# Performance work log

Measured on AMD Instinct MI355X. Metric: run time of the kernel, lower is better.

Reference implementation:

```python
import jax, jax.numpy as jnp
import numpy as np

IN_C, OUT_C, K, N_FILTERS, STRIDE, PAD = 256, 512, 3, 64, 1, 1


def setup_inputs() -> dict:
    key = jax.random.key(0)
    kx, kw, kb, krw, krb = jax.random.split(key, 5)
    fan_in = IN_C * K * K
    bound = 1.0 / np.sqrt(fan_in)
    x = jax.random.normal(kx, (32, IN_C, 56, 56), dtype=jnp.float32)
    weight = jax.random.uniform(kw, (OUT_C, IN_C, K, K), minval=-bound, maxval=bound, dtype=jnp.float32)
    bias = jax.random.uniform(kb, (OUT_C,), minval=-bound, maxval=bound, dtype=jnp.float32)
    rbound = 1.0 / np.sqrt(IN_C)
    router_w = jax.random.uniform(krw, (OUT_C, IN_C), minval=-rbound, maxval=rbound, dtype=jnp.float32)
    router_b = jax.random.uniform(krb, (OUT_C,), minval=-rbound, maxval=rbound, dtype=jnp.float32)
    return {"x": x, "weight": weight, "bias": bias, "router_w": router_w, "router_b": router_b}


def reference(x, weight, bias, router_w, router_b):
    B = x.shape[0]
    # router: global avg pool -> linear -> top-k channel mask
    pooled = jnp.mean(x, axis=(2, 3))                      # [B, IN_C]
    router_out = pooled @ router_w.T + router_b            # [B, OUT_C]
    _, top_idx = jax.lax.top_k(router_out, N_FILTERS)      # [B, k]
    mask = jnp.zeros((B, OUT_C), dtype=x.dtype).at[jnp.arange(B)[:, None], top_idx].set(1.0)
    # dense conv2d
    conv = jax.lax.conv_general_dilated(
        x, weight, window_strides=(STRIDE, STRIDE), padding=[(PAD, PAD), (PAD, PAD)],
        dimension_numbers=("NCHW", "OIHW", "NCHW"))
    conv = conv + bias[None, :, None, None]
    return conv * mask[:, :, None, None]
```

## Files before the change

### kernel.cpp

```cpp
#include <hip/hip_runtime.h>

#define IN_C   256
#define OUT_C  512
#define WIDTH  56
#define HW     3136
#define KTOT   2304
#define NF     64
#define NU     448
#define NB     32
#define NGRP   8
#define TN     64
#define NTILE  49
#define SROWS  192

typedef __bf16 bf16x8 __attribute__((ext_vector_type(8)));
typedef float  f32x4  __attribute__((ext_vector_type(4)));

__global__ __launch_bounds__(256) void xpose_kernel(const float* __restrict__ x,
                                                    __bf16* __restrict__ xT,
                                                    float* __restrict__ partial) {
    int id = blockIdx.x;
    int b = id / NTILE, tile = id - b * NTILE;
    int ptile = tile * TN;
    int tid = threadIdx.x;
    __shared__ float tl[64][65];
    __shared__ float plsum[IN_C];
    const float* xb  = x + (size_t)b * IN_C * HW + ptile;
    __bf16*      xtb = xT + ((size_t)b * HW + ptile) * IN_C;
    int pxq  = tid & 15;
    int rowi = tid >> 4;
    int px   = tid >> 2;
    int icq  = tid & 3;
    for (int chunk = 0; chunk < 4; ++chunk) {
        #pragma unroll
        for (int r = 0; r < 4; ++r) {
            int icL = r * 16 + rowi;
            int ic  = chunk * 64 + icL;
            float4 v = *(const float4*)(xb + (size_t)ic * HW + pxq * 4);
            *(float4*)&tl[icL][pxq * 4] = v;
            float s = v.x + v.y + v.z + v.w;
            s += __shfl_down(s, 8, 16);
            s += __shfl_down(s, 4, 16);
            s += __shfl_down(s, 2, 16);
            s += __shfl_down(s, 1, 16);
            if (pxq == 0) plsum[ic] = s;
        }
        __syncthreads();
        bf16x8 o0, o1;
        #pragma unroll
        for (int k = 0; k < 8; ++k) o0[k] = (__bf16)tl[icq * 16 + k][px];
        #pragma unroll
        for (int k = 0; k < 8; ++k) o1[k] = (__bf16)tl[icq * 16 + 8 + k][px];
        __bf16* dst = xtb + (size_t)px * IN_C + chunk * 64 + icq * 16;
        *(bf16x8*)dst = o0;
        *(bf16x8*)(dst + 8) = o1;
        __syncthreads();
    }
    partial[(size_t)id * IN_C + tid] = plsum[tid];
}

__global__ __launch_bounds__(256) void wfrag_kernel(const float* __restrict__ w,
                                                    __bf16* __restrict__ wf) {
    int oc = blockIdx.x;
    __shared__ float sm[KTOT];
    const float* src = w + (size_t)oc * KTOT;
    int tid = threadIdx.x;
    #pragma unroll
    for (int k = 0; k < 9; ++k) sm[k * 256 + tid] = src[k * 256 + tid];
    __syncthreads();
    __bf16* dst = wf + (size_t)oc * KTOT;
    for (int C = tid; C < 288; C += 256) {
        int d0  = C * 8;
        int icg = d0 / 288;
        int rem = d0 - icg * 288;
        int tap = rem >> 5, icl0 = rem & 31;
        bf16x8 o;
        #pragma unroll
        for (int j = 0; j < 8; ++j)
            o[j] = (__bf16)sm[(icg * 32 + icl0 + j) * 9 + tap];
        *(bf16x8*)&dst[d0] = o;
    }
}

__global__ __launch_bounds__(512) void router_kernel(const float* __restrict__ partial,
                                                     const float* __restrict__ rw,
                                                     const float* __restrict__ rb,
                                                     int* __restrict__ sel,
                                                     int* __restrict__ unsel) {
    int b = blockIdx.x;
    __shared__ float p[IN_C];
    __shared__ float v[OUT_C];
    __shared__ int   scount, ucount;
    int t = threadIdx.x;
    if (t < IN_C) {
        float s = 0.f;
        const float* pb = partial + (size_t)b * NTILE * IN_C + t;
        for (int k = 0; k < NTILE; ++k) s += pb[k * IN_C];
        p[t] = s * (1.0f / HW);
    }
    if (t == 0) { scount = 0; ucount = 0; }
    __syncthreads();
    int w = t >> 6, lane = t & 63;
    float4 pl = *(const float4*)&p[lane * 4];
    for (int k = 0; k < 64; ++k) {
        int oc = w * 64 + k;
        float4 wv = *(const float4*)&rw[(size_t)oc * IN_C + lane * 4];
        float d = pl.x * wv.x + pl.y * wv.y + pl.z * wv.z + pl.w * wv.w;
        #pragma unroll
        for (int off = 32; off > 0; off >>= 1) d += __shfl_down(d, off, 64);
        if (lane == 0) v[oc] = d + rb[oc];
    }
    __syncthreads();
    float acc = v[t];
    int cnt = 0;
    for (int j = 0; j < OUT_C; ++j) {
        float o = v[j];
        cnt += (o > acc) || (o == acc && j < t);
    }
    if (cnt < NF) {
        int pos = atomicAdd(&scount, 1);
        sel[b * NF + pos] = t;
    } else {
        int pos = atomicAdd(&ucount, 1);
        unsel[b * NU + pos] = t;
    }
}

__global__ __launch_bounds__(256) void acomp_kernel(const __bf16* __restrict__ wf,
                                                    const int* __restrict__ sel,
                                                    __bf16* __restrict__ A) {
    int blk = blockIdx.x;
    int b = blk >> 3, part = blk & 7;
    __shared__ int s[NF];
    int tid = threadIdx.x;
    if (tid < NF) s[tid] = sel[b * NF + tid];
    __syncthreads();
    __bf16* dst = A + (size_t)b * (NF * KTOT);
    #pragma unroll
    for (int c = part * 9; c < part * 9 + 9; ++c) {
        int C = c * 256 + tid;
        int icl8 = C & 3, oc = (C >> 2) & 63, gt = C >> 8;
        bf16x8 vv = *(const bf16x8*)&wf[(size_t)s[oc] * KTOT + gt * 32 + icl8 * 8];
        *(bf16x8*)&dst[(size_t)C * 8] = vv;
    }
}

__global__ __launch_bounds__(256, 2) void conv_kernel(const __bf16* __restrict__ xT,
                                                      const __bf16* __restrict__ Ac,
                                                      const float* __restrict__ bias,
                                                      const int* __restrict__ sel,
                                                      const int* __restrict__ unsel,
                                                      float* __restrict__ out) {
    int id   = blockIdx.x;
    int xcd  = id & 7, slot = id >> 3;
    int bq   = slot / NTILE;
    int tile = slot - bq * NTILE;
    int b    = xcd * 4 + bq;
    int ptile = tile * TN;

    int tid  = threadIdx.x;
    int lane = tid & 63, w = tid >> 6;
    int fm   = lane & 15, fq = lane >> 4;
    int mi2  = w >> 1,  s2 = w & 1;

    __shared__ __bf16 xlds[2][SROWS * 32];
    __shared__ int    selLds[NF];

    size_t outb = (size_t)b * OUT_C * HW;
    const __bf16* xtb = xT + (size_t)b * HW * IN_C;
    const __bf16* ab  = Ac + (size_t)b * (NF * KTOT);

    if (tid < NF) selLds[tid] = sel[b * NF + tid];

    {
        const int* ub = unsel + b * NU;
        f32x4 z = {0.f, 0.f, 0.f, 0.f};
        int lq = tid & 15;
        for (int u = tid >> 4; u < NU; u += 16) {
            int oc = ub[u];
            __builtin_nontemporal_store(z, (f32x4*)(out + outb + (size_t)oc * HW + ptile) + lq);
        }
    }

    const __bf16* sga[3];
    #pragma unroll
    for (int rnd = 0; rnd < 3; ++rnd) {
        int row = rnd * 64 + w * 16 + (lane >> 2);
        int cc  = (lane & 3) ^ ((row >> 1) & 3);
        int gp  = ptile - 57 + row;
        gp = gp < 0 ? 0 : (gp > HW - 1 ? HW - 1 : gp);
        sga[rnd] = xtb + (size_t)gp * IN_C + cc * 8;
    }

#define STAGE(buf, g) { \
    _Pragma("unroll") \
    for (int rnd = 0; rnd < 3; ++rnd) \
        __builtin_amdgcn_global_load_lds( \
            (const __attribute__((address_space(1))) void*)(sga[rnd] + (g) * 32), \
            (__attribute__((address_space(3))) void*)&xlds[buf][(rnd * 64 + w * 16) * 32], \
            16, 0, 0); }

    int pp[2], poh[2], pow_[2];
    #pragma unroll
    for (int sl = 0; sl < 2; ++sl) {
        int p = ptile + (s2 * 2 + sl) * 16 + fm;
        pp[sl]   = p;
        poh[sl]  = p / WIDTH;
        pow_[sl] = p - poh[sl] * WIDTH;
    }

    f32x4 acc[2][2] = {};

    STAGE(0, 0);
    __syncthreads();

    #pragma unroll 1
    for (int g = 0; g < NGRP; ++g) {
        int cur = g & 1;
        bf16x8 af[2][9];
        const __bf16* agp = ab + (size_t)(g * 9) * 2048;
        #pragma unroll
        for (int t9 = 0; t9 < 9; ++t9) {
            #pragma unroll
            for (int m = 0; m < 2; ++m)
                af[m][t9] = *(const bf16x8*)(agp + (size_t)t9 * 2048
                                             + ((mi2 * 2 + m) * 16 + fm) * 32 + fq * 8);
        }
        if (g < NGRP - 1) STAGE(cur ^ 1, g + 1);
        #pragma unroll
        for (int t9 = 0; t9 < 9; ++t9) {
            const int r = t9 / 3, c = t9 - 3 * r;
            const int shift = (r - 1) * WIDTH + (c - 1);
            #pragma unroll
            for (int sl = 0; sl < 2; ++sl) {
                int row = (s2 * 2 + sl) * 16 + fm + 57 + shift;
                int ohr = poh[sl] + r - 1, owc = pow_[sl] + c - 1;
                bool ok = ((unsigned)ohr < 56u) && ((unsigned)owc < 56u);
                int sw = fq ^ ((row >> 1) & 3);
                bf16x8 bfr = *(const bf16x8*)&xlds[cur][row * 32 + sw * 8];
                bf16x8 zz = {};
                bfr = ok ? bfr : zz;
                acc[0][sl] = __builtin_amdgcn_mfma_f32_16x16x32_bf16(af[0][t9], bfr, acc[0][sl], 0, 0, 0);
                acc[1][sl] = __builtin_amdgcn_mfma_f32_16x16x32_bf16(af[1][t9], bfr, acc[1][sl], 0, 0, 0);
            }
        }
        __syncthreads();
    }

    #pragma unroll
    for (int m = 0; m < 2; ++m) {
        int mi = mi2 * 2 + m;
        #pragma unroll
        for (int reg = 0; reg < 4; ++reg) {
            int oc = selLds[mi * 16 + fq * 4 + reg];
            float bs = bias[oc];
            float* orow = out + outb + (size_t)oc * HW;
            #pragma unroll
            for (int sl = 0; sl < 2; ++sl)
                __builtin_nontemporal_store(acc[m][sl][reg] + bs, &orow[pp[sl]]);
        }
    }
#undef STAGE
}

extern "C" void kernel_launch(void* const* d_in, const int* in_sizes, int n_in,
                              void* d_out, int out_size, void* d_ws, size_t ws_size,
                              hipStream_t stream) {
    (void)in_sizes; (void)n_in; (void)ws_size; (void)out_size;
    const float* x        = (const float*)d_in[0];
    const float* weight   = (const float*)d_in[1];
    const float* bias     = (const float*)d_in[2];
    const float* router_w = (const float*)d_in[3];
    const float* router_b = (const float*)d_in[4];
    float* out = (float*)d_out;

    char* ws = (char*)d_ws;
    __bf16* Acomp   = (__bf16*)ws;
    float*  partial = (float*)ws;
    __bf16* wfb     = (__bf16*)(ws + 0x900000);
    int*    sel     = (int*)(ws + 0xB40000);
    int*    unsel   = (int*)(ws + 0xB42000);
    __bf16* xT      = (__bf16*)(ws + 0xB50000);

    xpose_kernel <<<NB * NTILE, 256, 0, stream>>>(x, xT, partial);
    wfrag_kernel <<<OUT_C,      256, 0, stream>>>(weight, wfb);
    router_kernel<<<NB,         512, 0, stream>>>(partial, router_w, router_b, sel, unsel);
    acomp_kernel <<<NB * 8,     256, 0, stream>>>(wfb, sel, Acomp);
    conv_kernel  <<<NTILE * NB, 256, 0, stream>>>(xT, Acomp, bias, sel, unsel, out);
}
```

Before: 430.7 us.

## Fuse prep and router kernels, register-staged LDS loads, streamed A fragments

Merges the transpose and weight-reformat kernels into one launch, and merges routing with A-compaction, replacing atomics with a deterministic prefix scan. Each of the 8 compaction blocks per batch recomputes the router. In the conv kernel, the async global-to-LDS staging becomes register loads followed by LDS stores, and A fragments are double-buffered per tap instead of all 9 being preloaded. Launch bounds rise to 4 waves per SIMD to raise occupancy. The aims are fewer launches and lower register pressure, at the cost of redundant router work and less overlap of global loads with MFMA.

```diff
diff --git a/kernel.cpp b/kernel.cpp
--- a/kernel.cpp
+++ b/kernel.cpp
@@ -16,94 +16,98 @@
 typedef __bf16 bf16x8 __attribute__((ext_vector_type(8)));
 typedef float  f32x4  __attribute__((ext_vector_type(4)));
 
-__global__ __launch_bounds__(256) void xpose_kernel(const float* __restrict__ x,
-                                                    __bf16* __restrict__ xT,
-                                                    float* __restrict__ partial) {
-    int id = blockIdx.x;
-    int b = id / NTILE, tile = id - b * NTILE;
-    int ptile = tile * TN;
+__global__ __launch_bounds__(256) void prep_kernel(const float* __restrict__ x,
+                                                   __bf16* __restrict__ xT,
+                                                   float* __restrict__ partial,
+                                                   const float* __restrict__ wsrc,
+                                                   __bf16* __restrict__ wf) {
+    __shared__ float smem[64 * 65 + IN_C];
+    int id  = blockIdx.x;
     int tid = threadIdx.x;
-    __shared__ float tl[64][65];
-    __shared__ float plsum[IN_C];
-    const float* xb  = x + (size_t)b * IN_C * HW + ptile;
-    __bf16*      xtb = xT + ((size_t)b * HW + ptile) * IN_C;
-    int pxq  = tid & 15;
-    int rowi = tid >> 4;
-    int px   = tid >> 2;
-    int icq  = tid & 3;
-    for (int chunk = 0; chunk < 4; ++chunk) {
+    if (id < NB * NTILE) {
+        float (*tl)[65] = (float (*)[65])smem;
+        float* plsum = smem + 64 * 65;
+        int b = id / NTILE, tile = id - b * NTILE;
+        int ptile = tile * TN;
+        const float* xb  = x + (size_t)b * IN_C * HW + ptile;
+        __bf16*      xtb = xT + ((size_t)b * HW + ptile) * IN_C;
+        int pxq  = tid & 15;
+        int rowi = tid >> 4;
+        int px   = tid >> 2;
+        int icq  = tid & 3;
+        for (int chunk = 0; chunk < 4; ++chunk) {
+            #pragma unroll
+            for (int r = 0; r < 4; ++r) {
+                int icL = r * 16 + rowi;
+                int ic  = chunk * 64 + icL;
+                float4 v = *(const float4*)(xb + (size_t)ic * HW + pxq * 4);
+                *(float4*)&tl[icL][pxq * 4] = v;
+                float s = v.x + v.y + v.z + v.w;
+                s += __shfl_down(s, 8, 16);
+                s += __shfl_down(s, 4, 16);
+                s += __shfl_down(s, 2, 16);
+                s += __shfl_down(s, 1, 16);
+                if (pxq == 0) plsum[ic] = s;
+            }
+            __syncthreads();
+            bf16x8 o0, o1;
+            #pragma unroll
+            for (int k = 0; k < 8; ++k) o0[k] = (__bf16)tl[icq * 16 + k][px];
+            #pragma unroll
+            for (int k = 0; k < 8; ++k) o1[k] = (__bf16)tl[icq * 16 + 8 + k][px];
+            __bf16* dst = xtb + (size_t)px * IN_C + chunk * 64 + icq * 16;
+            *(bf16x8*)dst = o0;
+            *(bf16x8*)(dst + 8) = o1;
+            __syncthreads();
+        }
+        partial[(size_t)id * IN_C + tid] = plsum[tid];
+    } else {
+        int oc = id - NB * NTILE;
+        float* sm = smem;
+        const float* src = wsrc + (size_t)oc * KTOT;
         #pragma unroll
-        for (int r = 0; r < 4; ++r) {
-            int icL = r * 16 + rowi;
-            int ic  = chunk * 64 + icL;
-            float4 v = *(const float4*)(xb + (size_t)ic * HW + pxq * 4);
-            *(float4*)&tl[icL][pxq * 4] = v;
-            float s = v.x + v.y + v.z + v.w;
-            s += __shfl_down(s, 8, 16);
-            s += __shfl_down(s, 4, 16);
-            s += __shfl_down(s, 2, 16);
-            s += __shfl_down(s, 1, 16);
-            if (pxq == 0) plsum[ic] = s;
-        }
+        for (int k = 0; k < 9; ++k) sm[k * 256 + tid] = src[k * 256 + tid];
         __syncthreads();
-        bf16x8 o0, o1;
-        #pragma unroll
-        for (int k = 0; k < 8; ++k) o0[k] = (__bf16)tl[icq * 16 + k][px];
-        #pragma unroll
-        for (int k = 0; k < 8; ++k) o1[k] = (__bf16)tl[icq * 16 + 8 + k][px];
-        __bf16* dst = xtb + (size_t)px * IN_C + chunk * 64 + icq * 16;
-        *(bf16x8*)dst = o0;
-        *(bf16x8*)(dst + 8) = o1;
-        __syncthreads();
-    }
-    partial[(size_t)id * IN_C + tid] = plsum[tid];
+        __bf16* dst = wf + (size_t)oc * KTOT;
+        for (int C = tid; C < 288; C += 256) {
+            int d0  = C * 8;
+            int icg = d0 / 288;
+            int rem = d0 - icg * 288;
+            int tap = rem >> 5, icl0 = rem & 31;
+            bf16x8 o;
+            #pragma unroll
+            for (int j = 0; j < 8; ++j)
+                o[j] = (__bf16)sm[(icg * 32 + icl0 + j) * 9 + tap];
+            *(bf16x8*)&dst[d0] = o;
+        }
+    }
 }
 
-__global__ __launch_bounds__(256) void wfrag_kernel(const float* __restrict__ w,
-                                                    __bf16* __restrict__ wf) {
-    int oc = blockIdx.x;
-    __shared__ float sm[KTOT];
-    const float* src = w + (size_t)oc * KTOT;
-    int tid = threadIdx.x;
-    #pragma unroll
-    for (int k = 0; k < 9; ++k) sm[k * 256 + tid] = src[k * 256 + tid];
-    __syncthreads();
-    __bf16* dst = wf + (size_t)oc * KTOT;
-    for (int C = tid; C < 288; C += 256) {
-        int d0  = C * 8;
-        int icg = d0 / 288;
-        int rem = d0 - icg * 288;
-        int tap = rem >> 5, icl0 = rem & 31;
-        bf16x8 o;
-        #pragma unroll
-        for (int j = 0; j < 8; ++j)
-            o[j] = (__bf16)sm[(icg * 32 + icl0 + j) * 9 + tap];
-        *(bf16x8*)&dst[d0] = o;
-    }
-}
-
-__global__ __launch_bounds__(512) void router_kernel(const float* __restrict__ partial,
-                                                     const float* __restrict__ rw,
-                                                     const float* __restrict__ rb,
-                                                     int* __restrict__ sel,
-                                                     int* __restrict__ unsel) {
-    int b = blockIdx.x;
+__global__ __launch_bounds__(256) void route_acomp_kernel(const float* __restrict__ partial,
+                                                          const float* __restrict__ rw,
+                                                          const float* __restrict__ rb,
+                                                          const __bf16* __restrict__ wf,
+                                                          int* __restrict__ sel,
+                                                          int* __restrict__ unsel,
+                                                          __bf16* __restrict__ A) {
+    int blk = blockIdx.x;
+    int b = blk >> 3, part = blk & 7;
     __shared__ float p[IN_C];
     __shared__ float v[OUT_C];
-    __shared__ int   scount, ucount;
+    __shared__ int   fl[OUT_C];
+    __shared__ int   sL[NF];
     int t = threadIdx.x;
-    if (t < IN_C) {
+    {
         float s = 0.f;
         const float* pb = partial + (size_t)b * NTILE * IN_C + t;
         for (int k = 0; k < NTILE; ++k) s += pb[k * IN_C];
         p[t] = s * (1.0f / HW);
     }
-    if (t == 0) { scount = 0; ucount = 0; }
     __syncthreads();
     int w = t >> 6, lane = t & 63;
     float4 pl = *(const float4*)&p[lane * 4];
-    for (int k = 0; k < 64; ++k) {
-        int oc = w * 64 + k;
+    for (int k = 0; k < 128; ++k) {
+        int oc = w * 128 + k;
         float4 wv = *(const float4*)&rw[(size_t)oc * IN_C + lane * 4];
         float d = pl.x * wv.x + pl.y * wv.y + pl.z * wv.z + pl.w * wv.w;
         #pragma unroll
@@ -111,41 +115,42 @@
         if (lane == 0) v[oc] = d + rb[oc];
     }
     __syncthreads();
-    float acc = v[t];
-    int cnt = 0;
-    for (int j = 0; j < OUT_C; ++j) {
-        float o = v[j];
-        cnt += (o > acc) || (o == acc && j < t);
-    }
-    if (cnt < NF) {
-        int pos = atomicAdd(&scount, 1);
-        sel[b * NF + pos] = t;
-    } else {
-        int pos = atomicAdd(&ucount, 1);
-        unsel[b * NU + pos] = t;
+    #pragma unroll
+    for (int rep = 0; rep < 2; ++rep) {
+        int oc = rep * 256 + t;
+        float acc = v[oc];
+        int cnt = 0;
+        for (int j = 0; j < OUT_C; ++j) {
+            float o = v[j];
+            cnt += (o > acc) || (o == acc && j < oc);
+        }
+        fl[oc] = (cnt < NF) ? 1 : 0;
+    }
+    __syncthreads();
+    #pragma unroll
+    for (int rep = 0; rep < 2; ++rep) {
+        int oc = rep * 256 + t;
+        int spos = 0;
+        for (int j = 0; j < oc; ++j) spos += fl[j];
+        if (fl[oc]) {
+            sL[spos] = oc;
+            if (part == 0) sel[b * NF + spos] = oc;
+        } else if (part == 0) {
+            unsel[b * NU + (oc - spos)] = oc;
+        }
+    }
+    __syncthreads();
+    __bf16* dst = A + (size_t)b * (NF * KTOT);
+    #pragma unroll
+    for (int c = part * 9; c < part * 9 + 9; ++c) {
+        int C = c * 256 + t;
+        int icl8 = C & 3, oc = (C >> 2) & 63, gt = C >> 8;
+        bf16x8 vv = *(const bf16x8*)&wf[(size_t)sL[oc] * KTOT + gt * 32 + icl8 * 8];
+        *(bf16x8*)&dst[(size_t)C * 8] = vv;
     }
 }
 
-__global__ __launch_bounds__(256) void acomp_kernel(const __bf16* __restrict__ wf,
-                                                    const int* __restrict__ sel,
-                                                    __bf16* __restrict__ A) {
-    int blk = blockIdx.x;
-    int b = blk >> 3, part = blk & 7;
-    __shared__ int s[NF];
-    int tid = threadIdx.x;
-    if (tid < NF) s[tid] = sel[b * NF + tid];
-    __syncthreads();
-    __bf16* dst = A + (size_t)b * (NF * KTOT);
-    #pragma unroll
-    for (int c = part * 9; c < part * 9 + 9; ++c) {
-        int C = c * 256 + tid;
-        int icl8 = C & 3, oc = (C >> 2) & 63, gt = C >> 8;
-        bf16x8 vv = *(const bf16x8*)&wf[(size_t)s[oc] * KTOT + gt * 32 + icl8 * 8];
-        *(bf16x8*)&dst[(size_t)C * 8] = vv;
-    }
-}
-
-__global__ __launch_bounds__(256, 2) void conv_kernel(const __bf16* __restrict__ xT,
+__global__ __launch_bounds__(256, 4) void conv_kernel(const __bf16* __restrict__ xT,
                                                       const __bf16* __restrict__ Ac,
                                                       const float* __restrict__ bias,
                                                       const int* __restrict__ sel,
@@ -170,6 +175,22 @@
     const __bf16* xtb = xT + (size_t)b * HW * IN_C;
     const __bf16* ab  = Ac + (size_t)b * (NF * KTOT);
 
+    const __bf16* sga[3];
+    int           srow[3];
+    #pragma unroll
+    for (int rnd = 0; rnd < 3; ++rnd) {
+        int row = rnd * 64 + w * 16 + (lane >> 2);
+        int cc  = (lane & 3) ^ ((row >> 1) & 3);
+        int gp  = ptile - 57 + row;
+        gp = gp < 0 ? 0 : (gp > HW - 1 ? HW - 1 : gp);
+        sga[rnd]  = xtb + (size_t)gp * IN_C + cc * 8;
+        srow[rnd] = row;
+    }
+
+    uint4 xr[3];
+    #pragma unroll
+    for (int rnd = 0; rnd < 3; ++rnd) xr[rnd] = *(const uint4*)(sga[rnd]);
+
     if (tid < NF) selLds[tid] = sel[b * NF + tid];
 
     {
@@ -182,23 +203,15 @@
         }
     }
 
-    const __bf16* sga[3];
-    #pragma unroll
-    for (int rnd = 0; rnd < 3; ++rnd) {
-        int row = rnd * 64 + w * 16 + (lane >> 2);
-        int cc  = (lane & 3) ^ ((row >> 1) & 3);
-        int gp  = ptile - 57 + row;
-        gp = gp < 0 ? 0 : (gp > HW - 1 ? HW - 1 : gp);
-        sga[rnd] = xtb + (size_t)gp * IN_C + cc * 8;
-    }
-
-#define STAGE(buf, g) { \
-    _Pragma("unroll") \
-    for (int rnd = 0; rnd < 3; ++rnd) \
-        __builtin_amdgcn_global_load_lds( \
-            (const __attribute__((address_space(1))) void*)(sga[rnd] + (g) * 32), \
-            (__attribute__((address_space(3))) void*)&xlds[buf][(rnd * 64 + w * 16) * 32], \
-            16, 0, 0); }
+    #pragma unroll
+    for (int rnd = 0; rnd < 3; ++rnd)
+        *(uint4*)&xlds[0][srow[rnd] * 32 + (lane & 3) * 8] = xr[rnd];
+    __syncthreads();
+
+    const __bf16* pA[2];
+    #pragma unroll
+    for (int m = 0; m < 2; ++m)
+        pA[m] = ab + (size_t)((mi2 * 2 + m) * 16 + fm) * 32 + fq * 8;
 
     int pp[2], poh[2], pow_[2];
     #pragma unroll
@@ -211,38 +224,43 @@
 
     f32x4 acc[2][2] = {};
 
-    STAGE(0, 0);
-    __syncthreads();
-
     #pragma unroll 1
     for (int g = 0; g < NGRP; ++g) {
         int cur = g & 1;
-        bf16x8 af[2][9];
-        const __bf16* agp = ab + (size_t)(g * 9) * 2048;
+        const size_t gb = (size_t)(g * 9) * 2048;
+        bf16x8 afp[2][2];
+        afp[0][0] = *(const bf16x8*)(pA[0] + gb);
+        afp[0][1] = *(const bf16x8*)(pA[1] + gb);
         #pragma unroll
         for (int t9 = 0; t9 < 9; ++t9) {
-            #pragma unroll
-            for (int m = 0; m < 2; ++m)
-                af[m][t9] = *(const bf16x8*)(agp + (size_t)t9 * 2048
-                                             + ((mi2 * 2 + m) * 16 + fm) * 32 + fq * 8);
-        }
-        if (g < NGRP - 1) STAGE(cur ^ 1, g + 1);
-        #pragma unroll
-        for (int t9 = 0; t9 < 9; ++t9) {
-            const int r = t9 / 3, c = t9 - 3 * r;
-            const int shift = (r - 1) * WIDTH + (c - 1);
+            const int pc = t9 & 1;
+            if (t9 < 8) {
+                afp[pc ^ 1][0] = *(const bf16x8*)(pA[0] + gb + (size_t)(t9 + 1) * 2048);
+                afp[pc ^ 1][1] = *(const bf16x8*)(pA[1] + gb + (size_t)(t9 + 1) * 2048);
+            }
+            const int kr = t9 / 3, kc = t9 - 3 * kr;
+            const int shift = (kr - 1) * WIDTH + (kc - 1);
             #pragma unroll
             for (int sl = 0; sl < 2; ++sl) {
                 int row = (s2 * 2 + sl) * 16 + fm + 57 + shift;
-                int ohr = poh[sl] + r - 1, owc = pow_[sl] + c - 1;
+                int ohr = poh[sl] + kr - 1, owc = pow_[sl] + kc - 1;
                 bool ok = ((unsigned)ohr < 56u) && ((unsigned)owc < 56u);
                 int sw = fq ^ ((row >> 1) & 3);
                 bf16x8 bfr = *(const bf16x8*)&xlds[cur][row * 32 + sw * 8];
                 bf16x8 zz = {};
                 bfr = ok ? bfr : zz;
-                acc[0][sl] = __builtin_amdgcn_mfma_f32_16x16x32_bf16(af[0][t9], bfr, acc[0][sl], 0, 0, 0);
-                acc[1][sl] = __builtin_amdgcn_mfma_f32_16x16x32_bf16(af[1][t9], bfr, acc[1][sl], 0, 0, 0);
+                acc[0][sl] = __builtin_amdgcn_mfma_f32_16x16x32_bf16(afp[pc][0], bfr, acc[0][sl], 0, 0, 0);
+                acc[1][sl] = __builtin_amdgcn_mfma_f32_16x16x32_bf16(afp[pc][1], bfr, acc[1][sl], 0, 0, 0);
             }
+        }
+        if (g < NGRP - 1) {
+            __builtin_amdgcn_sched_barrier(0);
+            #pragma unroll
+            for (int rnd = 0; rnd < 3; ++rnd)
+                xr[rnd] = *(const uint4*)(sga[rnd] + (size_t)(g + 1) * 32);
+            #pragma unroll
+            for (int rnd = 0; rnd < 3; ++rnd)
+                *(uint4*)&xlds[cur ^ 1][srow[rnd] * 32 + (lane & 3) * 8] = xr[rnd];
         }
         __syncthreads();
     }
@@ -260,7 +278,6 @@
                 __builtin_nontemporal_store(acc[m][sl][reg] + bs, &orow[pp[sl]]);
         }
     }
-#undef STAGE
 }
 
 extern "C" void kernel_launch(void* const* d_in, const int* in_sizes, int n_in,
@@ -275,16 +292,15 @@
     float* out = (float*)d_out;
 
     char* ws = (char*)d_ws;
-    __bf16* Acomp   = (__bf16*)ws;
     float*  partial = (float*)ws;
-    __bf16* wfb     = (__bf16*)(ws + 0x900000);
-    int*    sel     = (int*)(ws + 0xB40000);
-    int*    unsel   = (int*)(ws + 0xB42000);
-    __bf16* xT      = (__bf16*)(ws + 0xB50000);
-
-    xpose_kernel <<<NB * NTILE, 256, 0, stream>>>(x, xT, partial);
-    wfrag_kernel <<<OUT_C,      256, 0, stream>>>(weight, wfb);
-    router_kernel<<<NB,         512, 0, stream>>>(partial, router_w, router_b, sel, unsel);
-    acomp_kernel <<<NB * 8,     256, 0, stream>>>(wfb, sel, Acomp);
-    conv_kernel  <<<NTILE * NB, 256, 0, stream>>>(xT, Acomp, bias, sel, unsel, out);
+    __bf16* wfb     = (__bf16*)(ws + 0x190000);
+    int*    sel     = (int*)(ws + 0x400000);
+    int*    unsel   = (int*)(ws + 0x402000);
+    __bf16* Acomp   = (__bf16*)(ws + 0x410000);
+    __bf16* xT      = (__bf16*)(ws + 0xD10000);
+
+    prep_kernel       <<<NB * NTILE + OUT_C, 256, 0, stream>>>(x, xT, partial, weight, wfb);
+    route_acomp_kernel<<<NB * 8,             256, 0, stream>>>(partial, router_w, router_b,
+                                                               wfb, sel, unsel, Acomp);
+    conv_kernel       <<<NTILE * NB,         256, 0, stream>>>(xT, Acomp, bias, sel, unsel, out);
 }
```

After: 470.9 us. 1.09x slower.
